# Optimization experiments

Measured on AMD Instinct MI355X. Metric: run time of the kernel, lower is better.

Reference implementation:

```python
import jax, jax.numpy as jnp
import numpy as np

B, P, K_NB, D, H = 4, 1024, 32, 768, 12
S = P + 1
HD = D // H  # 64

def _ln(x, w, b):
    m = jnp.mean(x, -1, keepdims=True)
    v = jnp.var(x, -1, keepdims=True)
    return (x - m) / jnp.sqrt(v + 1e-5) * w + b

def setup_inputs() -> dict:
    key = jax.random.key(0)
    ks = jax.random.split(key, 8)
    w = lambda k, sh: jax.random.normal(k, sh, jnp.float32) * 0.02
    return {
        'x': jax.random.normal(ks[0], (B, S, D), jnp.float32),
        'routes': jax.random.randint(ks[1], (P, K_NB), 0, P, dtype=jnp.int32),
        'qkv_w': w(ks[2], (D, 3 * D)), 'qkv_b': jnp.zeros((3 * D,), jnp.float32),
        'proj_w': w(ks[3], (D, D)), 'proj_b': jnp.zeros((D,), jnp.float32),
        'ln1_w': jnp.ones((D,), jnp.float32), 'ln1_b': jnp.zeros((D,), jnp.float32),
        'ln2_w': jnp.ones((D,), jnp.float32), 'ln2_b': jnp.zeros((D,), jnp.float32),
        'mlp_w1': w(ks[4], (D, 4 * D)), 'mlp_b1': jnp.zeros((4 * D,), jnp.float32),
        'mlp_w2': w(ks[5], (4 * D, D)), 'mlp_b2': jnp.zeros((D,), jnp.float32),
    }

def reference(x, routes, qkv_w, qkv_b, proj_w, proj_b, ln1_w, ln1_b,
              ln2_w, ln2_b, mlp_w1, mlp_b1, mlp_w2, mlp_b2):
    scale = HD ** -0.5
    xn = _ln(x, ln1_w, ln1_b)
    qkv = (xn @ qkv_w + qkv_b).reshape(B, S, 3, H, HD).transpose(2, 0, 3, 1, 4)
    Q, Kt, V = qkv[0], qkv[1], qkv[2]  # each [B,H,S,HD]
    # CLS token: full dense attention over all S tokens
    sc = jnp.einsum('bhqd,bhkd->bhqk', Q[:, :, :1], Kt) * scale
    oc = jnp.einsum('bhqk,bhkd->bhqd', jax.nn.softmax(sc, -1), V)  # [B,H,1,HD]
    # patch tokens: sparse attention over k routed neighbors
    r = routes + 1  # shift past CLS (buffer routes_shifted)
    Kg = Kt[:, :, r, :]  # [B,H,P,k,HD] gathered keys
    Vg = V[:, :, r, :]   # [B,H,P,k,HD] gathered values
    sp = jnp.einsum('bhpd,bhpkd->bhpk', Q[:, :, 1:], Kg) * scale
    op = jnp.einsum('bhpk,bhpkd->bhpd', jax.nn.softmax(sp, -1), Vg)
    out = jnp.concatenate([oc, op], axis=2).transpose(0, 2, 1, 3).reshape(B, S, D)
    x = x + (out @ proj_w + proj_b)
    h = _ln(x, ln2_w, ln2_b)
    h = jax.nn.gelu(h @ mlp_w1 + mlp_b1, approximate=False) @ mlp_w2 + mlp_b2
    return x + h
```

## Files before the change

kernel.cpp:

```cpp
#include <hip/hip_runtime.h>
#include <hip/hip_bf16.h>

using bf16 = __hip_bfloat16;
using s8v  = __attribute__((ext_vector_type(8))) short;
using f4v  = __attribute__((ext_vector_type(4))) float;

constexpr int B_   = 4;
constexpr int P_   = 1024;
constexpr int KNB  = 32;
constexpr int D_   = 768;
constexpr int H_   = 12;
constexpr int S_   = P_ + 1;
constexpr int M_   = B_ * S_;
constexpr int MPAD = 4224;

#define DEVI static __device__ __forceinline__
#define WAITVM(N) asm volatile("s_waitcnt vmcnt(" #N ")" ::: "memory")
#define MEMFENCE  asm volatile("" ::: "memory")

DEVI float b2f_lo(unsigned u) { return __builtin_bit_cast(float, u << 16); }
DEVI float b2f_hi(unsigned u) { return __builtin_bit_cast(float, u & 0xffff0000u); }
DEVI unsigned short f2bu(float f) {
  return __builtin_bit_cast(unsigned short, __float2bfloat16(f));
}

DEVI void wt_conv_dev(const float* __restrict__ W, bf16* __restrict__ Wt,
                      int KK, int NN, int idx, int tid, float (*t)[33]) {
  int nbn = NN >> 5;
  int bk = (idx / nbn) * 32, bn = (idx % nbn) * 32;
  int tx = tid & 31, ty = tid >> 5;
#pragma unroll
  for (int i = 0; i < 32; i += 8)
    t[ty + i][tx] = W[(size_t)(bk + ty + i) * NN + bn + tx];
  __syncthreads();
#pragma unroll
  for (int i = 0; i < 32; i += 8)
    Wt[(size_t)(bn + ty + i) * KK + bk + tx] = __float2bfloat16(t[tx][ty + i]);
}

DEVI void ln_dev(const float* __restrict__ xr, const float* __restrict__ w,
                 const float* __restrict__ b, bf16* __restrict__ orow,
                 int t, float* sm, float* sv) {
  float v0 = xr[t], v1 = xr[t + 256], v2 = xr[t + 512];
  float s = v0 + v1 + v2;
  float ss = v0 * v0 + v1 * v1 + v2 * v2;
#pragma unroll
  for (int o = 32; o; o >>= 1) { s += __shfl_xor(s, o); ss += __shfl_xor(ss, o); }
  if ((t & 63) == 0) { sm[t >> 6] = s; sv[t >> 6] = ss; }
  __syncthreads();
  float S = sm[0] + sm[1] + sm[2] + sm[3];
  float SS = sv[0] + sv[1] + sv[2] + sv[3];
  float mean = S * (1.f / D_);
  float var  = SS * (1.f / D_) - mean * mean;
  float inv  = rsqrtf(var + 1e-5f);
  orow[t]       = __float2bfloat16((v0 - mean) * inv * w[t]       + b[t]);
  orow[t + 256] = __float2bfloat16((v1 - mean) * inv * w[t + 256] + b[t + 256]);
  orow[t + 512] = __float2bfloat16((v2 - mean) * inv * w[t + 512] + b[t + 512]);
}

__global__ __launch_bounds__(256)
void prep(const float* __restrict__ qkv_w, const float* __restrict__ proj_w,
          const float* __restrict__ mlp_w1, const float* __restrict__ mlp_w2,
          bf16* qkvw_t, bf16* projw_t, bf16* mlpw1_t, bf16* mlpw2_t,
          const float* __restrict__ x, const float* __restrict__ ln1_w,
          const float* __restrict__ ln1_b, bf16* xnA) {
  __shared__ float t[32][33];
  __shared__ float sm[4], sv[4];
  int idx = blockIdx.x, tid = threadIdx.x;
  if (idx < 1728)       wt_conv_dev(qkv_w,  qkvw_t,  768,  2304, idx,        tid, t);
  else if (idx < 2304)  wt_conv_dev(proj_w, projw_t, 768,  768,  idx - 1728, tid, t);
  else if (idx < 4608)  wt_conv_dev(mlp_w1, mlpw1_t, 768,  3072, idx - 2304, tid, t);
  else if (idx < 6912)  wt_conv_dev(mlp_w2, mlpw2_t, 3072, 768,  idx - 4608, tid, t);
  else {
    int row = idx - 6912;
    ln_dev(x + (size_t)row * D_, ln1_w, ln1_b, xnA + (size_t)row * D_, tid, sm, sv);
  }
}

template<int N, int KSTRIDE, int KCHUNK, int MODE>
__global__ __launch_bounds__(256)
void gemm_bf16(const bf16* __restrict__ A, const bf16* __restrict__ Bt,
               const float* __restrict__ bias, void* __restrict__ dst) {
  constexpr int BM   = 64;
  constexpr int MR   = 2;
  constexpr int TN   = N / 128;
  constexpr int NBLK = (MPAD / BM) * TN;
  __shared__ bf16 ldsA[3][BM * 32];
  __shared__ bf16 ldsB[3][128 * 32];

  int bid = blockIdx.x;
  constexpr int NQ = NBLK >> 3, NR = NBLK & 7;
  int xcd = bid & 7, off = bid >> 3;
  int swz = (xcd < NR ? xcd * (NQ + 1) : NR * (NQ + 1) + (xcd - NR) * NQ) + off;
  const int tm = swz / TN, tn = swz % TN;
  const int kbase = blockIdx.y * KCHUNK;

  const int tid = threadIdx.x;
  const int wid = tid >> 6, lane = tid & 63;
  const int wr = wid >> 1, wc = wid & 1;

  auto stage = [&](int bufi, int step) {
    const int k0 = kbase + step * 32;
    {
      int c = wid * 64 + lane;
      int r = c >> 2, slot = c & 3;
      int gs = slot ^ ((r >> 1) & 3);
      const bf16* ga = A + (size_t)(tm * BM + r) * KSTRIDE + k0 + gs * 8;
      bf16* la = &ldsA[bufi][(wid * 64 + lane) * 8];
      __builtin_amdgcn_global_load_lds(
          (__attribute__((address_space(1))) void*)ga,
          (__attribute__((address_space(3))) void*)la, 16, 0, 0);
    }
#pragma unroll
    for (int i = 0; i < 2; ++i) {
      int c = wid * 64 + i * 256 + lane;
      int r = c >> 2, slot = c & 3;
      int gs = slot ^ ((r >> 1) & 3);
      const bf16* ga = Bt + (size_t)(tn * 128 + r) * KSTRIDE + k0 + gs * 8;
      bf16* la = &ldsB[bufi][(wid * 64 + i * 256) * 8];
      __builtin_amdgcn_global_load_lds(
          (__attribute__((address_space(1))) void*)ga,
          (__attribute__((address_space(3))) void*)la, 16, 0, 0);
    }
  };

  f4v acc[MR][4] = {};
  const int nk = KCHUNK / 32;

  stage(0, 0); stage(1, 1);

#pragma unroll 3
  for (int kt = 0; kt < nk; ++kt) {
    if (kt < nk - 1) WAITVM(3);
    else             WAITVM(0);
    __builtin_amdgcn_s_barrier();
    MEMFENCE;
    if (kt + 2 < nk) stage((kt + 2) % 3, kt + 2);

    const int cur = kt % 3;
    s8v af[MR], bfv[4];
#pragma unroll
    for (int m = 0; m < MR; ++m) {
      int row = wr * 32 + m * 16 + (lane & 15);
      int slot = (lane >> 4) ^ ((row >> 1) & 3);
      af[m] = *(const s8v*)&ldsA[cur][row * 32 + slot * 8];
    }
#pragma unroll
    for (int n = 0; n < 4; ++n) {
      int row = wc * 64 + n * 16 + (lane & 15);
      int slot = (lane >> 4) ^ ((row >> 1) & 3);
      bfv[n] = *(const s8v*)&ldsB[cur][row * 32 + slot * 8];
    }
#pragma unroll
    for (int m = 0; m < MR; ++m)
#pragma unroll
      for (int n = 0; n < 4; ++n)
        acc[m][n] = __builtin_amdgcn_mfma_f32_16x16x32_bf16(af[m], bfv[n], acc[m][n], 0, 0, 0);
  }

#pragma unroll
  for (int m = 0; m < MR; ++m)
#pragma unroll
    for (int n = 0; n < 4; ++n)
#pragma unroll
      for (int j = 0; j < 4; ++j) {
        int row = tm * 64 + wr * 32 + m * 16 + (lane >> 4) * 4 + j;
        int col = tn * 128 + wc * 64 + n * 16 + (lane & 15);
        float v = acc[m][n][j];
        if (MODE == 0) {
          if (row < M_) {
            float val = v + bias[col];
            int which = col / 768, rem2 = col % 768;
            int bb = row / S_, s = row % S_;
            ((bf16*)dst)[((size_t)(which * B_ + bb) * S_ + s) * 768 + rem2] =
                __float2bfloat16(val);
          }
        } else if (MODE == 2) {
          if (row < M_) {
            float val = v + bias[col];
            val = 0.5f * val * (1.f + erff(val * 0.70710678f));
            ((bf16*)dst)[(size_t)row * N + col] = __float2bfloat16(val);
          }
        } else {
          bf16* p = (bf16*)dst + (size_t)blockIdx.y * MPAD * N;
          p[(size_t)row * N + col] = __float2bfloat16(v);
        }
      }
}

__global__ __launch_bounds__(256)
void projfix(const bf16* __restrict__ part, const float* __restrict__ x,
             const float* __restrict__ pbias, const float* __restrict__ lnw,
             const float* __restrict__ lnb, float* __restrict__ out,
             bf16* __restrict__ h2) {
  int row = blockIdx.x, t = threadIdx.x;
  const bf16* p0 = part + (size_t)row * D_;
  const bf16* p1 = part + (size_t)MPAD * D_ + (size_t)row * D_;
  const float* xr = x + (size_t)row * D_;
  float v[3];
#pragma unroll
  for (int i = 0; i < 3; ++i) {
    int c = t + i * 256;
    v[i] = xr[c] + pbias[c] + __bfloat162float(p0[c]) + __bfloat162float(p1[c]);
  }
  float* orow = out + (size_t)row * D_;
#pragma unroll
  for (int i = 0; i < 3; ++i) orow[t + i * 256] = v[i];
  float s = v[0] + v[1] + v[2];
  float ss = v[0] * v[0] + v[1] * v[1] + v[2] * v[2];
#pragma unroll
  for (int o = 32; o; o >>= 1) { s += __shfl_xor(s, o); ss += __shfl_xor(ss, o); }
  __shared__ float sm[4], sv[4];
  if ((t & 63) == 0) { sm[t >> 6] = s; sv[t >> 6] = ss; }
  __syncthreads();
  float S = sm[0] + sm[1] + sm[2] + sm[3];
  float SS = sv[0] + sv[1] + sv[2] + sv[3];
  float mean = S * (1.f / D_);
  float var  = SS * (1.f / D_) - mean * mean;
  float inv  = rsqrtf(var + 1e-5f);
  bf16* hrow = h2 + (size_t)row * D_;
#pragma unroll
  for (int i = 0; i < 3; ++i) {
    int c = t + i * 256;
    hrow[c] = __float2bfloat16((v[i] - mean) * inv * lnw[c] + lnb[c]);
  }
}

__global__ __launch_bounds__(256)
void reduceK(const bf16* __restrict__ part, const float* __restrict__ bias,
             float* __restrict__ out) {
  int i = blockIdx.x * 256 + threadIdx.x;
  ushort4 a = ((const ushort4*)part)[i];
  ushort4 b = ((const ushort4*)(part + (size_t)MPAD * 768))[i];
  float4 s = ((const float4*)out)[i];
  int col = (i * 4) % D_;
  float4 bv = *(const float4*)&bias[col];
  float4 o;
  o.x = s.x + bv.x + b2f_lo((unsigned)a.x << 16 >> 16 << 16 >> 16 | 0) ;
  o.x = s.x + bv.x + __bfloat162float(__hip_bfloat16_raw{a.x}) + __bfloat162float(__hip_bfloat16_raw{b.x});
  o.y = s.y + bv.y + __bfloat162float(__hip_bfloat16_raw{a.y}) + __bfloat162float(__hip_bfloat16_raw{b.y});
  o.z = s.z + bv.z + __bfloat162float(__hip_bfloat16_raw{a.z}) + __bfloat162float(__hip_bfloat16_raw{b.z});
  o.w = s.w + bv.w + __bfloat162float(__hip_bfloat16_raw{a.w}) + __bfloat162float(__hip_bfloat16_raw{b.w});
  ((float4*)out)[i] = o;
}

__global__ __launch_bounds__(256)
void attn_kernel(const bf16* __restrict__ QKV, const int* __restrict__ routes,
                 bf16* __restrict__ out) {
  __shared__ float qf[64];
  __shared__ float sc[S_];
  __shared__ float red[4];
  __shared__ float pv[4][64];

  if (blockIdx.x < 12288) {
    int unit = blockIdx.x * 4 + (threadIdx.x >> 6);
    int lane = threadIdx.x & 63;
    int h = unit % H_;
    int bp = unit / H_;
    int p = bp % P_, b = bp / P_;

    int k = lane & 31, hi = lane >> 5;
    int r = routes[p * KNB + k] + 1;

    const bf16* Qp = QKV + ((size_t)(0 * B_ + b) * S_ + (p + 1)) * D_ + h * 64 + hi * 32;
    const bf16* Kb = QKV + ((size_t)(1 * B_ + b) * S_) * D_;
    const bf16* Vb = QKV + ((size_t)(2 * B_ + b) * S_) * D_;

    const uint4* q4 = (const uint4*)Qp;
    const uint4* k4 = (const uint4*)(Kb + (size_t)r * D_ + h * 64 + hi * 32);
    float dot = 0.f;
#pragma unroll
    for (int i = 0; i < 4; ++i) {
      uint4 qv = q4[i], kv = k4[i];
      dot += b2f_lo(kv.x) * b2f_lo(qv.x) + b2f_hi(kv.x) * b2f_hi(qv.x)
           + b2f_lo(kv.y) * b2f_lo(qv.y) + b2f_hi(kv.y) * b2f_hi(qv.y)
           + b2f_lo(kv.z) * b2f_lo(qv.z) + b2f_hi(kv.z) * b2f_hi(qv.z)
           + b2f_lo(kv.w) * b2f_lo(qv.w) + b2f_hi(kv.w) * b2f_hi(qv.w);
    }
    dot += __shfl_xor(dot, 32);
    float scv = dot * 0.125f;

    float mx = scv;
#pragma unroll
    for (int o = 16; o; o >>= 1) mx = fmaxf(mx, __shfl_xor(mx, o));
    float w = __expf(scv - mx);
    float sum = w;
#pragma unroll
    for (int o = 16; o; o >>= 1) sum += __shfl_xor(sum, o);
    float inv = 1.f / sum;

    int c = lane & 7, kr0 = lane >> 3;
    float acc[8] = {};
#pragma unroll
    for (int j = 0; j < 4; ++j) {
      int kj = (kr0 & 7) + 8 * j;
      float wj = __shfl(w, kj);
      int rj = __shfl(r, kj);
      uint4 vv = *(const uint4*)(Vb + (size_t)rj * D_ + h * 64 + c * 8);
      acc[0] += wj * b2f_lo(vv.x); acc[1] += wj * b2f_hi(vv.x);
      acc[2] += wj * b2f_lo(vv.y); acc[3] += wj * b2f_hi(vv.y);
      acc[4] += wj * b2f_lo(vv.z); acc[5] += wj * b2f_hi(vv.z);
      acc[6] += wj * b2f_lo(vv.w); acc[7] += wj * b2f_hi(vv.w);
    }
#pragma unroll
    for (int s = 8; s < 64; s <<= 1)
#pragma unroll
      for (int d = 0; d < 8; ++d) acc[d] += __shfl_xor(acc[d], s);

    if (lane < 8) {
      s8v o;
#pragma unroll
      for (int d = 0; d < 8; ++d) o[d] = (short)f2bu(acc[d] * inv);
      *(s8v*)(out + ((size_t)(b * S_ + p + 1)) * D_ + h * 64 + c * 8) = o;
    }
  } else {
    int bh = blockIdx.x - 12288;
    int b = bh / H_, h = bh % H_;
    const bf16* q  = QKV + ((size_t)(0 * B_ + b) * S_) * D_ + h * 64;
    const bf16* Kr = QKV + ((size_t)(1 * B_ + b) * S_) * D_ + h * 64;
    const bf16* Vr = QKV + ((size_t)(2 * B_ + b) * S_) * D_ + h * 64;
    int t = threadIdx.x;
    if (t < 64) qf[t] = __bfloat162float(q[t]);
    __syncthreads();
    for (int kk = t; kk < S_; kk += 256) {
      const uint4* k4 = (const uint4*)(Kr + (size_t)kk * D_);
      float s = 0.f;
#pragma unroll
      for (int i = 0; i < 8; ++i) {
        uint4 kv = k4[i];
        const float* q8 = &qf[i * 8];
        s += b2f_lo(kv.x) * q8[0] + b2f_hi(kv.x) * q8[1]
           + b2f_lo(kv.y) * q8[2] + b2f_hi(kv.y) * q8[3]
           + b2f_lo(kv.z) * q8[4] + b2f_hi(kv.z) * q8[5]
           + b2f_lo(kv.w) * q8[6] + b2f_hi(kv.w) * q8[7];
      }
      sc[kk] = s * 0.125f;
    }
    __syncthreads();
    float mx = -1e30f;
    for (int kk = t; kk < S_; kk += 256) mx = fmaxf(mx, sc[kk]);
#pragma unroll
    for (int o = 32; o; o >>= 1) mx = fmaxf(mx, __shfl_xor(mx, o));
    if ((t & 63) == 0) red[t >> 6] = mx;
    __syncthreads();
    float M = fmaxf(fmaxf(red[0], red[1]), fmaxf(red[2], red[3]));
    __syncthreads();
    float sum = 0.f;
    for (int kk = t; kk < S_; kk += 256) { float e = __expf(sc[kk] - M); sc[kk] = e; sum += e; }
#pragma unroll
    for (int o = 32; o; o >>= 1) sum += __shfl_xor(sum, o);
    if ((t & 63) == 0) red[t >> 6] = sum;
    __syncthreads();
    float L = red[0] + red[1] + red[2] + red[3];
    float inv = 1.f / L;
    int d = t & 63, kg = t >> 6;
    float acc = 0.f;
    for (int kk = kg; kk < S_; kk += 4)
      acc += sc[kk] * __bfloat162float(Vr[(size_t)kk * D_ + d]);
    pv[kg][d] = acc;
    __syncthreads();
    if (t < 64) {
      float ov = (pv[0][t] + pv[1][t] + pv[2][t] + pv[3][t]) * inv;
      out[(size_t)(b * S_) * D_ + h * 64 + t] = __float2bfloat16(ov);
    }
  }
}

extern "C" void kernel_launch(void* const* d_in, const int* in_sizes, int n_in,
                              void* d_out, int out_size, void* d_ws, size_t ws_size,
                              hipStream_t stream) {
  const float* x      = (const float*)d_in[0];
  const int*   routes = (const int*)d_in[1];
  const float* qkv_w  = (const float*)d_in[2];
  const float* qkv_b  = (const float*)d_in[3];
  const float* proj_w = (const float*)d_in[4];
  const float* proj_b = (const float*)d_in[5];
  const float* ln1_w  = (const float*)d_in[6];
  const float* ln1_b  = (const float*)d_in[7];
  const float* ln2_w  = (const float*)d_in[8];
  const float* ln2_b  = (const float*)d_in[9];
  const float* mlp_w1 = (const float*)d_in[10];
  const float* mlp_b1 = (const float*)d_in[11];
  const float* mlp_w2 = (const float*)d_in[12];
  const float* mlp_b2 = (const float*)d_in[13];
  float* out = (float*)d_out;

  bf16* qkvw_t  = (bf16*)d_ws;
  bf16* projw_t = qkvw_t + 2304 * 768;
  bf16* mlpw1_t = projw_t + 768 * 768;
  bf16* mlpw2_t = mlpw1_t + 3072 * 768;
  bf16* xnA     = mlpw2_t + 768 * 3072;
  bf16* qkvbuf  = xnA + (size_t)MPAD * 768;
  bf16* attn    = qkvbuf + (size_t)3 * B_ * S_ * 768;
  bf16* h2      = attn + (size_t)MPAD * 768;
  bf16* g       = xnA;
  bf16* projp   = xnA;
  bf16* mlp2p   = attn;

  prep<<<6912 + M_, 256, 0, stream>>>(qkv_w, proj_w, mlp_w1, mlp_w2,
                                      qkvw_t, projw_t, mlpw1_t, mlpw2_t,
                                      x, ln1_w, ln1_b, xnA);

  gemm_bf16<2304, 768, 768, 0><<<66 * 18, 256, 0, stream>>>(xnA, qkvw_t, qkv_b, qkvbuf);

  attn_kernel<<<12288 + B_ * H_, 256, 0, stream>>>(qkvbuf, routes, attn);

  gemm_bf16<768, 768, 384, 3><<<dim3(66 * 6, 2), 256, 0, stream>>>(attn, projw_t, nullptr, projp);

  projfix<<<M_, 256, 0, stream>>>(projp, x, proj_b, ln2_w, ln2_b, out, h2);

  gemm_bf16<3072, 768, 768, 2><<<66 * 24, 256, 0, stream>>>(h2, mlpw1_t, mlp_b1, g);

  gemm_bf16<768, 3072, 1536, 3><<<dim3(66 * 6, 2), 256, 0, stream>>>(g, mlpw2_t, nullptr, mlp2p);

  reduceK<<<(M_ * D_) / 1024, 256, 0, stream>>>(mlp2p, mlp_b2, out);
}
```

Baseline: 380.2 us.

## Use 128-row GEMM tiles with 4-deep pipeline and prefetch attention loads

The GEMM kernel now takes the M tile and pipeline depth as template parameters. The QKV and MLP1 GEMMs use 128x128 tiles with a 4-stage LDS pipeline and wait counts adjusted to match. This raises per-block data reuse and keeps more loads in flight, at the cost of fewer blocks and more LDS and registers per block. The attention kernel now issues its Q, K and gathered V loads together before computing, and puts the CLS blocks first in the grid so the long dense-attention blocks start early.

```diff
diff --git a/kernel.cpp b/kernel.cpp
--- a/kernel.cpp
+++ b/kernel.cpp
@@ -77,16 +77,16 @@
   }
 }
 
-template<int N, int KSTRIDE, int KCHUNK, int MODE>
+template<int BM, int DEPTH, int N, int KSTRIDE, int KCHUNK, int MODE>
 __global__ __launch_bounds__(256)
 void gemm_bf16(const bf16* __restrict__ A, const bf16* __restrict__ Bt,
                const float* __restrict__ bias, void* __restrict__ dst) {
-  constexpr int BM   = 64;
-  constexpr int MR   = 2;
+  constexpr int MR   = BM / 32;
+  constexpr int LPS  = BM / 64 + 2;
   constexpr int TN   = N / 128;
   constexpr int NBLK = (MPAD / BM) * TN;
-  __shared__ bf16 ldsA[3][BM * 32];
-  __shared__ bf16 ldsB[3][128 * 32];
+  __shared__ bf16 ldsA[DEPTH][BM * 32];
+  __shared__ bf16 ldsB[DEPTH][128 * 32];
 
   int bid = blockIdx.x;
   constexpr int NQ = NBLK >> 3, NR = NBLK & 7;
@@ -101,12 +101,13 @@
 
   auto stage = [&](int bufi, int step) {
     const int k0 = kbase + step * 32;
-    {
-      int c = wid * 64 + lane;
+#pragma unroll
+    for (int i = 0; i < BM / 64; ++i) {
+      int c = wid * 64 + i * 256 + lane;
       int r = c >> 2, slot = c & 3;
       int gs = slot ^ ((r >> 1) & 3);
       const bf16* ga = A + (size_t)(tm * BM + r) * KSTRIDE + k0 + gs * 8;
-      bf16* la = &ldsA[bufi][(wid * 64 + lane) * 8];
+      bf16* la = &ldsA[bufi][(wid * 64 + i * 256) * 8];
       __builtin_amdgcn_global_load_lds(
           (__attribute__((address_space(1))) void*)ga,
           (__attribute__((address_space(3))) void*)la, 16, 0, 0);
@@ -128,20 +129,35 @@
   const int nk = KCHUNK / 32;
 
   stage(0, 0); stage(1, 1);
-
-#pragma unroll 3
+  if constexpr (DEPTH == 4) stage(2, 2);
+
+#pragma unroll 4
   for (int kt = 0; kt < nk; ++kt) {
-    if (kt < nk - 1) WAITVM(3);
-    else             WAITVM(0);
+    const int rem = nk - kt;
+    if constexpr (DEPTH == 4) {
+      if (rem > 2) {
+        if constexpr (LPS == 4) WAITVM(8); else WAITVM(6);
+      } else if (rem == 2) {
+        if constexpr (LPS == 4) WAITVM(4); else WAITVM(3);
+      } else WAITVM(0);
+    } else {
+      if (rem > 1) {
+        if constexpr (LPS == 4) WAITVM(4); else WAITVM(3);
+      } else WAITVM(0);
+    }
     __builtin_amdgcn_s_barrier();
     MEMFENCE;
-    if (kt + 2 < nk) stage((kt + 2) % 3, kt + 2);
-
-    const int cur = kt % 3;
+    if constexpr (DEPTH == 4) {
+      if (kt + 3 < nk) stage((kt + 3) & 3, kt + 3);
+    } else {
+      if (kt + 2 < nk) stage((kt + 2) % 3, kt + 2);
+    }
+
+    const int cur = (DEPTH == 4) ? (kt & 3) : (kt % 3);
     s8v af[MR], bfv[4];
 #pragma unroll
     for (int m = 0; m < MR; ++m) {
-      int row = wr * 32 + m * 16 + (lane & 15);
+      int row = wr * (MR * 16) + m * 16 + (lane & 15);
       int slot = (lane >> 4) ^ ((row >> 1) & 3);
       af[m] = *(const s8v*)&ldsA[cur][row * 32 + slot * 8];
     }
@@ -164,7 +180,7 @@
     for (int n = 0; n < 4; ++n)
 #pragma unroll
       for (int j = 0; j < 4; ++j) {
-        int row = tm * 64 + wr * 32 + m * 16 + (lane >> 4) * 4 + j;
+        int row = tm * BM + wr * (MR * 16) + m * 16 + (lane >> 4) * 4 + j;
         int col = tn * 128 + wc * 64 + n * 16 + (lane & 15);
         float v = acc[m][n][j];
         if (MODE == 0) {
@@ -236,7 +252,6 @@
   int col = (i * 4) % D_;
   float4 bv = *(const float4*)&bias[col];
   float4 o;
-  o.x = s.x + bv.x + b2f_lo((unsigned)a.x << 16 >> 16 << 16 >> 16 | 0) ;
   o.x = s.x + bv.x + __bfloat162float(__hip_bfloat16_raw{a.x}) + __bfloat162float(__hip_bfloat16_raw{b.x});
   o.y = s.y + bv.y + __bfloat162float(__hip_bfloat16_raw{a.y}) + __bfloat162float(__hip_bfloat16_raw{b.y});
   o.z = s.z + bv.z + __bfloat162float(__hip_bfloat16_raw{a.z}) + __bfloat162float(__hip_bfloat16_raw{b.z});
@@ -252,8 +267,8 @@
   __shared__ float red[4];
   __shared__ float pv[4][64];
 
-  if (blockIdx.x < 12288) {
-    int unit = blockIdx.x * 4 + (threadIdx.x >> 6);
+  if (blockIdx.x >= 48) {
+    int unit = (blockIdx.x - 48) * 4 + (threadIdx.x >> 6);
     int lane = threadIdx.x & 63;
     int h = unit % H_;
     int bp = unit / H_;
@@ -268,14 +283,24 @@
 
     const uint4* q4 = (const uint4*)Qp;
     const uint4* k4 = (const uint4*)(Kb + (size_t)r * D_ + h * 64 + hi * 32);
+    int c = lane & 7, kr0 = lane >> 3;
+    uint4 qv[4], kv[4], vv[4];
+#pragma unroll
+    for (int i = 0; i < 4; ++i) { qv[i] = q4[i]; kv[i] = k4[i]; }
+#pragma unroll
+    for (int j = 0; j < 4; ++j) {
+      int kj = kr0 + 8 * j;
+      int rj = __shfl(r, kj);
+      vv[j] = *(const uint4*)(Vb + (size_t)rj * D_ + h * 64 + c * 8);
+    }
+
     float dot = 0.f;
 #pragma unroll
     for (int i = 0; i < 4; ++i) {
-      uint4 qv = q4[i], kv = k4[i];
-      dot += b2f_lo(kv.x) * b2f_lo(qv.x) + b2f_hi(kv.x) * b2f_hi(qv.x)
-           + b2f_lo(kv.y) * b2f_lo(qv.y) + b2f_hi(kv.y) * b2f_hi(qv.y)
-           + b2f_lo(kv.z) * b2f_lo(qv.z) + b2f_hi(kv.z) * b2f_hi(qv.z)
-           + b2f_lo(kv.w) * b2f_lo(qv.w) + b2f_hi(kv.w) * b2f_hi(qv.w);
+      dot += b2f_lo(kv[i].x) * b2f_lo(qv[i].x) + b2f_hi(kv[i].x) * b2f_hi(qv[i].x)
+           + b2f_lo(kv[i].y) * b2f_lo(qv[i].y) + b2f_hi(kv[i].y) * b2f_hi(qv[i].y)
+           + b2f_lo(kv[i].z) * b2f_lo(qv[i].z) + b2f_hi(kv[i].z) * b2f_hi(qv[i].z)
+           + b2f_lo(kv[i].w) * b2f_lo(qv[i].w) + b2f_hi(kv[i].w) * b2f_hi(qv[i].w);
     }
     dot += __shfl_xor(dot, 32);
     float scv = dot * 0.125f;
@@ -289,18 +314,15 @@
     for (int o = 16; o; o >>= 1) sum += __shfl_xor(sum, o);
     float inv = 1.f / sum;
 
-    int c = lane & 7, kr0 = lane >> 3;
     float acc[8] = {};
 #pragma unroll
     for (int j = 0; j < 4; ++j) {
-      int kj = (kr0 & 7) + 8 * j;
+      int kj = kr0 + 8 * j;
       float wj = __shfl(w, kj);
-      int rj = __shfl(r, kj);
-      uint4 vv = *(const uint4*)(Vb + (size_t)rj * D_ + h * 64 + c * 8);
-      acc[0] += wj * b2f_lo(vv.x); acc[1] += wj * b2f_hi(vv.x);
-      acc[2] += wj * b2f_lo(vv.y); acc[3] += wj * b2f_hi(vv.y);
-      acc[4] += wj * b2f_lo(vv.z); acc[5] += wj * b2f_hi(vv.z);
-      acc[6] += wj * b2f_lo(vv.w); acc[7] += wj * b2f_hi(vv.w);
+      acc[0] += wj * b2f_lo(vv[j].x); acc[1] += wj * b2f_hi(vv[j].x);
+      acc[2] += wj * b2f_lo(vv[j].y); acc[3] += wj * b2f_hi(vv[j].y);
+      acc[4] += wj * b2f_lo(vv[j].z); acc[5] += wj * b2f_hi(vv[j].z);
+      acc[6] += wj * b2f_lo(vv[j].w); acc[7] += wj * b2f_hi(vv[j].w);
     }
 #pragma unroll
     for (int s = 8; s < 64; s <<= 1)
@@ -314,7 +336,7 @@
       *(s8v*)(out + ((size_t)(b * S_ + p + 1)) * D_ + h * 64 + c * 8) = o;
     }
   } else {
-    int bh = blockIdx.x - 12288;
+    int bh = blockIdx.x;
     int b = bh / H_, h = bh % H_;
     const bf16* q  = QKV + ((size_t)(0 * B_ + b) * S_) * D_ + h * 64;
     const bf16* Kr = QKV + ((size_t)(1 * B_ + b) * S_) * D_ + h * 64;
@@ -401,17 +423,17 @@
                                       qkvw_t, projw_t, mlpw1_t, mlpw2_t,
                                       x, ln1_w, ln1_b, xnA);
 
-  gemm_bf16<2304, 768, 768, 0><<<66 * 18, 256, 0, stream>>>(xnA, qkvw_t, qkv_b, qkvbuf);
-
-  attn_kernel<<<12288 + B_ * H_, 256, 0, stream>>>(qkvbuf, routes, attn);
-
-  gemm_bf16<768, 768, 384, 3><<<dim3(66 * 6, 2), 256, 0, stream>>>(attn, projw_t, nullptr, projp);
+  gemm_bf16<128, 4, 2304, 768, 768, 0><<<33 * 18, 256, 0, stream>>>(xnA, qkvw_t, qkv_b, qkvbuf);
+
+  attn_kernel<<<48 + 12288, 256, 0, stream>>>(qkvbuf, routes, attn);
+
+  gemm_bf16<64, 3, 768, 768, 384, 3><<<dim3(66 * 6, 2), 256, 0, stream>>>(attn, projw_t, nullptr, projp);
 
   projfix<<<M_, 256, 0, stream>>>(projp, x, proj_b, ln2_w, ln2_b, out, h2);
 
-  gemm_bf16<3072, 768, 768, 2><<<66 * 24, 256, 0, stream>>>(h2, mlpw1_t, mlp_b1, g);
-
-  gemm_bf16<768, 3072, 1536, 3><<<dim3(66 * 6, 2), 256, 0, stream>>>(g, mlpw2_t, nullptr, mlp2p);
+  gemm_bf16<128, 4, 3072, 768, 768, 2><<<33 * 24, 256, 0, stream>>>(h2, mlpw1_t, mlp_b1, g);
+
+  gemm_bf16<64, 3, 768, 3072, 1536, 3><<<dim3(66 * 6, 2), 256, 0, stream>>>(g, mlpw2_t, nullptr, mlp2p);
 
   reduceK<<<(M_ * D_) / 1024, 256, 0, stream>>>(mlp2p, mlp_b2, out);
 }
```

After: 378.5 us. About the same (-0.4%).
